# Kernel optimization log

Hardware: AMD Instinct MI355X
Metric: run time of the kernel (lower is better)

## Reference

```python
import jax, jax.numpy as jnp
import numpy as np

DIM_IN = 512
HIDDEN = 512
DIM_OUT = 512
BATCH = 256

def _n_tri(d):
    return (d * d + d) // 2

def _quad_expand(x):
    # x: [B, D] -> [B, D + (D^2+D)/2] with upper-triu (incl diag) pairwise products
    d = x.shape[1]
    iu0, iu1 = np.triu_indices(d)  # static indices
    x_sq = x[:, iu0] * x[:, iu1]  # [B, n_tri] -- avoids materializing full outer
    return jnp.concatenate([x, x_sq], axis=-1)

def setup_inputs() -> dict:
    key = jax.random.key(0)
    k = jax.random.split(key, 5)
    f0 = DIM_IN + _n_tri(DIM_IN)
    f1 = HIDDEN + _n_tri(HIDDEN)
    s0 = 1.0 / np.sqrt(f0)
    s1 = 1.0 / np.sqrt(f1)
    return {
        "x": jax.random.normal(k[0], (BATCH, DIM_IN), dtype=jnp.float32),
        "W0": jax.random.uniform(k[1], (HIDDEN, f0), dtype=jnp.float32, minval=-s0, maxval=s0),
        "b0": jax.random.uniform(k[2], (HIDDEN,), dtype=jnp.float32, minval=-s0, maxval=s0),
        "W1": jax.random.uniform(k[3], (DIM_OUT, f1), dtype=jnp.float32, minval=-s1, maxval=s1),
        "b1": jax.random.uniform(k[4], (DIM_OUT,), dtype=jnp.float32, minval=-s1, maxval=s1),
    }

def reference(x, W0, b0, W1, b1):
    h = _quad_expand(x) @ W0.T + b0  # [B, HIDDEN]
    out = _quad_expand(h) @ W1.T + b1  # [B, DIM_OUT]
    return out
```

## Files before the change

kernel.cpp:

```cpp
#include <hip/hip_runtime.h>

typedef short s16x8 __attribute__((ext_vector_type(8)));
typedef float f32x4 __attribute__((ext_vector_type(4)));

#define DIM     512
#define BATCH   256
#define NTRI    131328
#define FDIM    131840
#define KBLOCKS 2060
#define BN      128
#define NTILES  4
#define CCH     64

__device__ __forceinline__ unsigned short f2bf(float f) {
  __bf16 h = (__bf16)f;
  return __builtin_bit_cast(unsigned short, h);
}
__device__ __forceinline__ float bf2f(unsigned short s) {
  union { unsigned u; float f; } v; v.u = (unsigned)s << 16; return v.f;
}
__device__ __forceinline__ unsigned pk2(float a, float b) {
  return (unsigned)f2bf(a) | ((unsigned)f2bf(b) << 16);
}
__device__ __forceinline__ int swz(int m) { return (m ^ (m >> 2)) & 7; }

__global__ void setup(unsigned* __restrict__ table, const float* __restrict__ x,
                      unsigned short* __restrict__ Xt) {
  int bid = blockIdx.x;
  if (bid < 512) {
    int i = bid;
    int base = i * DIM - (i * (i - 1)) / 2;
    int len = DIM - i;
    for (int t = threadIdx.x; t < len; t += blockDim.x)
      table[base + t] = ((unsigned)i << 16) | (unsigned)(i + t);
  } else {
    int t = (bid - 512) * blockDim.x + threadIdx.x;
    int r = t & (BATCH - 1);
    int c = t >> 8;
    Xt[c * BATCH + r] = f2bf(x[r * DIM + c]);
  }
}

__global__ __launch_bounds__(512)
void featgen(const unsigned* __restrict__ table,
             const unsigned short* __restrict__ Xt,
             uint4* __restrict__ Feat)
{
  const int kb = blockIdx.x;
  const int tid = threadIdx.x;
  const int s8 = tid >> 6;
  const int lane = tid & 63;
  const int f0 = kb * 64 + s8 * 8;
  uint4* out = Feat + ((size_t)kb * 8 + s8) * 256;

  if (f0 < DIM) {
    #pragma unroll
    for (int mb = 0; mb < 4; ++mb) {
      int m = mb * 64 + lane;
      unsigned short v[8];
      #pragma unroll
      for (int e = 0; e < 8; ++e) v[e] = Xt[(f0 + e) * BATCH + m];
      uint4 pk;
      pk.x = (unsigned)v[0] | ((unsigned)v[1] << 16);
      pk.y = (unsigned)v[2] | ((unsigned)v[3] << 16);
      pk.z = (unsigned)v[4] | ((unsigned)v[5] << 16);
      pk.w = (unsigned)v[6] | ((unsigned)v[7] << 16);
      out[m] = pk;
    }
  } else {
    int p0 = f0 - DIM;
    unsigned t0 = table[p0], t7 = table[p0 + 7];
    if ((t0 >> 16) == (t7 >> 16)) {
      int i = (int)(t0 >> 16), j0 = (int)(t0 & 0xffffu);
      #pragma unroll
      for (int mb = 0; mb < 4; ++mb) {
        int m = mb * 64 + lane;
        float xi = bf2f(Xt[i * BATCH + m]);
        float pr[8];
        #pragma unroll
        for (int e = 0; e < 8; ++e) pr[e] = xi * bf2f(Xt[(j0 + e) * BATCH + m]);
        out[m] = make_uint4(pk2(pr[0], pr[1]), pk2(pr[2], pr[3]),
                            pk2(pr[4], pr[5]), pk2(pr[6], pr[7]));
      }
    } else {
      unsigned tt[8];
      #pragma unroll
      for (int e = 0; e < 8; ++e) tt[e] = table[p0 + e];
      #pragma unroll
      for (int mb = 0; mb < 4; ++mb) {
        int m = mb * 64 + lane;
        float pr[8];
        #pragma unroll
        for (int e = 0; e < 8; ++e)
          pr[e] = bf2f(Xt[(tt[e] >> 16) * BATCH + m]) * bf2f(Xt[(tt[e] & 0xffffu) * BATCH + m]);
        out[m] = make_uint4(pk2(pr[0], pr[1]), pk2(pr[2], pr[3]),
                            pk2(pr[4], pr[5]), pk2(pr[6], pr[7]));
      }
    }
  }
}

__global__ __launch_bounds__(512, 2)
void qgemm(const uint4* __restrict__ Feat,
           const float* __restrict__ W,
           unsigned short* __restrict__ partial,
           int C)
{
  __shared__ unsigned short Ws[2][BN * 64];
  const int chunk = blockIdx.x % C;
  const int ntile = blockIdx.x / C;
  const int kb0 = (KBLOCKS * chunk) / C;
  const int kb1 = (KBLOCKS * (chunk + 1)) / C;
  const int n0 = ntile * BN;
  const int tid = threadIdx.x;
  const int lane = tid & 63;
  const int wave = tid >> 6;
  const int wm = wave & 3;
  const int wn = wave >> 2;
  const int lm = lane & 15;
  const int lk = lane >> 4;

  const int wr0 = tid >> 4;
  const int wc16 = tid & 15;

  f32x4 acc[4][4] = {};
  f32x4 wregC[4], wregN[4], wT[4];
  uint4 afrC[4][2], afrN[4][2];

  const float* wp0 = W + (size_t)(n0 + wr0) * FDIM + wc16 * 4;
  const size_t wrow32 = (size_t)32 * FDIM;
  const int abase = lk * 256 + wm * 64 + lm;

  auto loadA = [&](uint4 (*a)[2], int kb) {
    #pragma unroll
    for (int mf = 0; mf < 4; ++mf)
      #pragma unroll
      for (int ks = 0; ks < 2; ++ks)
        a[mf][ks] = Feat[(size_t)kb * 2048 + ks * 1024 + mf * 16 + abase];
  };
  auto loadWr = [&](f32x4* w, int kb) {
    #pragma unroll
    for (int it = 0; it < 4; ++it)
      w[it] = *(const f32x4*)(wp0 + it * wrow32 + (size_t)kb * 64);
  };
  auto storeWs = [&](int buf, const f32x4* w) {
    #pragma unroll
    for (int it = 0; it < 4; ++it) {
      int r = wr0 + it * 32;
      int slot = (wc16 >> 1) ^ swz(r);
      *(uint2*)((char*)&Ws[buf][0] + r * 128 + slot * 16 + (wc16 & 1) * 8) =
          make_uint2(pk2(w[it][0], w[it][1]), pk2(w[it][2], w[it][3]));
    }
  };
  auto compute = [&](int buf, uint4 (*a)[2]) {
    #pragma unroll
    for (int ks = 0; ks < 2; ++ks) {
      s16x8 bfr[4];
      #pragma unroll
      for (int nf = 0; nf < 4; ++nf) {
        int n = wn * 64 + nf * 16 + lm;
        int slot = (ks * 4 + lk) ^ swz(n);
        bfr[nf] = *(const s16x8*)((const char*)&Ws[buf][0] + n * 128 + slot * 16);
      }
      __builtin_amdgcn_s_setprio(1);
      #pragma unroll
      for (int mf = 0; mf < 4; ++mf)
        #pragma unroll
        for (int nf = 0; nf < 4; ++nf)
          acc[mf][nf] = __builtin_amdgcn_mfma_f32_16x16x32_bf16(
              __builtin_bit_cast(s16x8, a[mf][ks]), bfr[nf], acc[mf][nf], 0, 0, 0);
      __builtin_amdgcn_s_setprio(0);
    }
  };

  loadA(afrC, kb0);
  loadWr(wT, kb0);
  loadWr(wregC, min(kb0 + 1, KBLOCKS - 1));
  storeWs(kb0 & 1, wT);
  asm volatile("s_waitcnt lgkmcnt(0)" ::: "memory");
  __builtin_amdgcn_s_barrier();

  for (int kb = kb0; kb < kb1 - 1; ++kb) {
    const int buf = kb & 1;
    loadA(afrN, kb + 1);
    loadWr(wregN, min(kb + 2, KBLOCKS - 1));
    storeWs(buf ^ 1, wregC);
    compute(buf, afrC);
    asm volatile("s_waitcnt lgkmcnt(0)" ::: "memory");
    __builtin_amdgcn_s_barrier();
    #pragma unroll
    for (int mf = 0; mf < 4; ++mf) {
      afrC[mf][0] = afrN[mf][0]; afrC[mf][1] = afrN[mf][1];
    }
    #pragma unroll
    for (int it = 0; it < 4; ++it) wregC[it] = wregN[it];
  }

  compute((kb1 - 1) & 1, afrC);

  unsigned short* pout = partial + (size_t)chunk * (BATCH * DIM);
  #pragma unroll
  for (int mf = 0; mf < 4; ++mf) {
    #pragma unroll
    for (int nf = 0; nf < 4; ++nf) {
      int mrow = wm * 64 + mf * 16 + lk * 4;
      int ncol = n0 + wn * 64 + nf * 16 + lm;
      #pragma unroll
      for (int r = 0; r < 4; ++r)
        pout[(size_t)(mrow + r) * DIM + ncol] = f2bf(acc[mf][nf][r]);
    }
  }
}

__global__ void reduce_h(const unsigned short* __restrict__ partial, const float* __restrict__ bias,
                         unsigned short* __restrict__ Ht, int C) {
  int u = blockIdx.x * blockDim.x + threadIdx.x;
  int t8 = u * 8;
  int b = t8 >> 9;
  int o0 = t8 & (DIM - 1);
  float s[8];
  #pragma unroll
  for (int e = 0; e < 8; ++e) s[e] = bias[o0 + e];
  for (int c = 0; c < C; ++c) {
    uint4 v = *(const uint4*)(partial + (size_t)c * (BATCH * DIM) + t8);
    unsigned w[4] = {v.x, v.y, v.z, v.w};
    #pragma unroll
    for (int p = 0; p < 4; ++p) {
      s[2*p]   += bf2f((unsigned short)(w[p] & 0xffffu));
      s[2*p+1] += bf2f((unsigned short)(w[p] >> 16));
    }
  }
  #pragma unroll
  for (int e = 0; e < 8; ++e)
    Ht[(o0 + e) * BATCH + b] = f2bf(s[e]);
}

__global__ void reduce_out(const unsigned short* __restrict__ partial, const float* __restrict__ bias,
                           float* __restrict__ out, int C) {
  int u = blockIdx.x * blockDim.x + threadIdx.x;
  int t8 = u * 8;
  int o0 = t8 & (DIM - 1);
  float s[8];
  #pragma unroll
  for (int e = 0; e < 8; ++e) s[e] = bias[o0 + e];
  for (int c = 0; c < C; ++c) {
    uint4 v = *(const uint4*)(partial + (size_t)c * (BATCH * DIM) + t8);
    unsigned w[4] = {v.x, v.y, v.z, v.w};
    #pragma unroll
    for (int p = 0; p < 4; ++p) {
      s[2*p]   += bf2f((unsigned short)(w[p] & 0xffffu));
      s[2*p+1] += bf2f((unsigned short)(w[p] >> 16));
    }
  }
  f32x4 lo = {s[0], s[1], s[2], s[3]};
  f32x4 hi = {s[4], s[5], s[6], s[7]};
  *(f32x4*)(out + t8) = lo;
  *(f32x4*)(out + t8 + 4) = hi;
}

extern "C" void kernel_launch(void* const* d_in, const int* in_sizes, int n_in,
                              void* d_out, int out_size, void* d_ws, size_t ws_size,
                              hipStream_t stream) {
  const float* x  = (const float*)d_in[0];
  const float* W0 = (const float*)d_in[1];
  const float* b0 = (const float*)d_in[2];
  const float* W1 = (const float*)d_in[3];
  const float* b1 = (const float*)d_in[4];
  float* out = (float*)d_out;

  char* ws = (char*)d_ws;
  unsigned* table    = (unsigned*)ws;
  unsigned short* Xt = (unsigned short*)(ws + 525312);
  unsigned short* Ht = (unsigned short*)(ws + 787456);
  uint4* Feat        = (uint4*)(ws + 1049600);
  size_t feat_end    = 1049600 + (size_t)KBLOCKS * 32768;
  unsigned short* partial = (unsigned short*)(ws + feat_end);

  size_t avail = (ws_size > feat_end) ? (ws_size - feat_end) : 0;
  int C = (int)(avail / ((size_t)BATCH * DIM * sizeof(unsigned short)));
  if (C > CCH) C = CCH;
  if (C < 1)  C = 1;

  setup<<<dim3(1024), dim3(256), 0, stream>>>(table, x, Xt);

  featgen<<<dim3(KBLOCKS), dim3(512), 0, stream>>>(table, Xt, Feat);
  qgemm<<<dim3(NTILES * C), dim3(512), 0, stream>>>(Feat, W0, partial, C);
  reduce_h<<<dim3(64), dim3(256), 0, stream>>>(partial, b0, Ht, C);

  featgen<<<dim3(KBLOCKS), dim3(512), 0, stream>>>(table, Ht, Feat);
  qgemm<<<dim3(NTILES * C), dim3(512), 0, stream>>>(Feat, W1, partial, C);
  reduce_out<<<dim3(64), dim3(256), 0, stream>>>(partial, b1, out, C);
}
```

Measured before the change: 245.2 us.

## Fuse quadratic feature generation into GEMM with LDS-staged A tiles

Removes the separate featgen pass that wrote the expanded bf16 feature matrix (about 67MB) to global memory. The GEMM now computes the pairwise products on the fly from the transposed input and stages them into shared memory. Blocks grow to 1024 threads with 256-column N tiles and up to 128 K-chunks, so each A tile is generated once per two N tiles instead of being read four times. The cost is more ALU and gather work inside the GEMM loop, more LDS use and lower occupancy.

```diff
diff --git a/kernel.cpp b/kernel.cpp
--- a/kernel.cpp
+++ b/kernel.cpp
@@ -8,9 +8,9 @@
 #define NTRI    131328
 #define FDIM    131840
 #define KBLOCKS 2060
-#define BN      128
-#define NTILES  4
-#define CCH     64
+#define BNW     256
+#define NTILES  2
+#define CCH     128
 
 __device__ __forceinline__ unsigned short f2bf(float f) {
   __bf16 h = (__bf16)f;
@@ -23,6 +23,7 @@
   return (unsigned)f2bf(a) | ((unsigned)f2bf(b) << 16);
 }
 __device__ __forceinline__ int swz(int m) { return (m ^ (m >> 2)) & 7; }
+#define SB() __builtin_amdgcn_sched_barrier(0)
 
 __global__ void setup(unsigned* __restrict__ table, const float* __restrict__ x,
                       unsigned short* __restrict__ Xt) {
@@ -41,77 +42,20 @@
   }
 }
 
-__global__ __launch_bounds__(512)
-void featgen(const unsigned* __restrict__ table,
-             const unsigned short* __restrict__ Xt,
-             uint4* __restrict__ Feat)
-{
-  const int kb = blockIdx.x;
-  const int tid = threadIdx.x;
-  const int s8 = tid >> 6;
-  const int lane = tid & 63;
-  const int f0 = kb * 64 + s8 * 8;
-  uint4* out = Feat + ((size_t)kb * 8 + s8) * 256;
-
-  if (f0 < DIM) {
-    #pragma unroll
-    for (int mb = 0; mb < 4; ++mb) {
-      int m = mb * 64 + lane;
-      unsigned short v[8];
-      #pragma unroll
-      for (int e = 0; e < 8; ++e) v[e] = Xt[(f0 + e) * BATCH + m];
-      uint4 pk;
-      pk.x = (unsigned)v[0] | ((unsigned)v[1] << 16);
-      pk.y = (unsigned)v[2] | ((unsigned)v[3] << 16);
-      pk.z = (unsigned)v[4] | ((unsigned)v[5] << 16);
-      pk.w = (unsigned)v[6] | ((unsigned)v[7] << 16);
-      out[m] = pk;
-    }
-  } else {
-    int p0 = f0 - DIM;
-    unsigned t0 = table[p0], t7 = table[p0 + 7];
-    if ((t0 >> 16) == (t7 >> 16)) {
-      int i = (int)(t0 >> 16), j0 = (int)(t0 & 0xffffu);
-      #pragma unroll
-      for (int mb = 0; mb < 4; ++mb) {
-        int m = mb * 64 + lane;
-        float xi = bf2f(Xt[i * BATCH + m]);
-        float pr[8];
-        #pragma unroll
-        for (int e = 0; e < 8; ++e) pr[e] = xi * bf2f(Xt[(j0 + e) * BATCH + m]);
-        out[m] = make_uint4(pk2(pr[0], pr[1]), pk2(pr[2], pr[3]),
-                            pk2(pr[4], pr[5]), pk2(pr[6], pr[7]));
-      }
-    } else {
-      unsigned tt[8];
-      #pragma unroll
-      for (int e = 0; e < 8; ++e) tt[e] = table[p0 + e];
-      #pragma unroll
-      for (int mb = 0; mb < 4; ++mb) {
-        int m = mb * 64 + lane;
-        float pr[8];
-        #pragma unroll
-        for (int e = 0; e < 8; ++e)
-          pr[e] = bf2f(Xt[(tt[e] >> 16) * BATCH + m]) * bf2f(Xt[(tt[e] & 0xffffu) * BATCH + m]);
-        out[m] = make_uint4(pk2(pr[0], pr[1]), pk2(pr[2], pr[3]),
-                            pk2(pr[4], pr[5]), pk2(pr[6], pr[7]));
-      }
-    }
-  }
-}
-
-__global__ __launch_bounds__(512, 2)
-void qgemm(const uint4* __restrict__ Feat,
+__global__ __launch_bounds__(1024)
+void qgemm(const unsigned* __restrict__ table,
+           const unsigned short* __restrict__ Xt,
            const float* __restrict__ W,
            unsigned short* __restrict__ partial,
            int C)
 {
-  __shared__ unsigned short Ws[2][BN * 64];
+  __shared__ char As[2][8 * 4128];
+  __shared__ unsigned short Ws[2][BNW * 64];
   const int chunk = blockIdx.x % C;
   const int ntile = blockIdx.x / C;
   const int kb0 = (KBLOCKS * chunk) / C;
   const int kb1 = (KBLOCKS * (chunk + 1)) / C;
-  const int n0 = ntile * BN;
+  const int n0 = ntile * BNW;
   const int tid = threadIdx.x;
   const int lane = tid & 63;
   const int wave = tid >> 6;
@@ -122,81 +66,110 @@
 
   const int wr0 = tid >> 4;
   const int wc16 = tid & 15;
+  const int m = tid & 255;
+  const int gb = tid >> 8;
 
   f32x4 acc[4][4] = {};
-  f32x4 wregC[4], wregN[4], wT[4];
-  uint4 afrC[4][2], afrN[4][2];
+  f32x4 wrN[4];
 
   const float* wp0 = W + (size_t)(n0 + wr0) * FDIM + wc16 * 4;
-  const size_t wrow32 = (size_t)32 * FDIM;
-  const int abase = lk * 256 + wm * 64 + lm;
-
-  auto loadA = [&](uint4 (*a)[2], int kb) {
-    #pragma unroll
-    for (int mf = 0; mf < 4; ++mf)
-      #pragma unroll
-      for (int ks = 0; ks < 2; ++ks)
-        a[mf][ks] = Feat[(size_t)kb * 2048 + ks * 1024 + mf * 16 + abase];
+  const size_t wrow64 = (size_t)64 * FDIM;
+
+  auto fgen = [&](int kb, int g) -> uint4 {
+    int f0 = kb * 64 + g * 8;
+    if (f0 < DIM) {
+      unsigned short v[8];
+      #pragma unroll
+      for (int e = 0; e < 8; ++e) v[e] = Xt[(f0 + e) * BATCH + m];
+      return make_uint4((unsigned)v[0] | ((unsigned)v[1] << 16),
+                        (unsigned)v[2] | ((unsigned)v[3] << 16),
+                        (unsigned)v[4] | ((unsigned)v[5] << 16),
+                        (unsigned)v[6] | ((unsigned)v[7] << 16));
+    }
+    int p0 = f0 - DIM;
+    unsigned t0 = table[p0], t7 = table[p0 + 7];
+    float pr[8];
+    if ((t0 >> 16) == (t7 >> 16)) {
+      float xi = bf2f(Xt[(t0 >> 16) * BATCH + m]);
+      int j0 = (int)(t0 & 0xffffu);
+      #pragma unroll
+      for (int e = 0; e < 8; ++e) pr[e] = xi * bf2f(Xt[(j0 + e) * BATCH + m]);
+    } else {
+      #pragma unroll
+      for (int e = 0; e < 8; ++e) {
+        unsigned ij = table[p0 + e];
+        pr[e] = bf2f(Xt[(ij >> 16) * BATCH + m]) * bf2f(Xt[(ij & 0xffffu) * BATCH + m]);
+      }
+    }
+    return make_uint4(pk2(pr[0], pr[1]), pk2(pr[2], pr[3]),
+                      pk2(pr[4], pr[5]), pk2(pr[6], pr[7]));
+  };
+  auto stageA = [&](int kb, int buf) {
+    #pragma unroll
+    for (int p = 0; p < 2; ++p) {
+      int g = gb + 4 * p;
+      uint4 v = fgen(kb, g);
+      *(uint4*)(&As[buf][g * 4128 + m * 16]) = v;
+    }
   };
   auto loadWr = [&](f32x4* w, int kb) {
     #pragma unroll
     for (int it = 0; it < 4; ++it)
-      w[it] = *(const f32x4*)(wp0 + it * wrow32 + (size_t)kb * 64);
+      w[it] = *(const f32x4*)(wp0 + it * wrow64 + (size_t)kb * 64);
   };
   auto storeWs = [&](int buf, const f32x4* w) {
     #pragma unroll
     for (int it = 0; it < 4; ++it) {
-      int r = wr0 + it * 32;
+      int r = wr0 + it * 64;
       int slot = (wc16 >> 1) ^ swz(r);
       *(uint2*)((char*)&Ws[buf][0] + r * 128 + slot * 16 + (wc16 & 1) * 8) =
           make_uint2(pk2(w[it][0], w[it][1]), pk2(w[it][2], w[it][3]));
     }
   };
-  auto compute = [&](int buf, uint4 (*a)[2]) {
+  auto compute = [&](int buf) {
     #pragma unroll
     for (int ks = 0; ks < 2; ++ks) {
-      s16x8 bfr[4];
+      s16x8 bfr[4], afr[4];
       #pragma unroll
       for (int nf = 0; nf < 4; ++nf) {
         int n = wn * 64 + nf * 16 + lm;
         int slot = (ks * 4 + lk) ^ swz(n);
         bfr[nf] = *(const s16x8*)((const char*)&Ws[buf][0] + n * 128 + slot * 16);
       }
+      #pragma unroll
+      for (int mf = 0; mf < 4; ++mf)
+        afr[mf] = *(const s16x8*)(&As[buf][(ks * 4 + lk) * 4128 + (wm * 64 + mf * 16 + lm) * 16]);
       __builtin_amdgcn_s_setprio(1);
       #pragma unroll
       for (int mf = 0; mf < 4; ++mf)
         #pragma unroll
         for (int nf = 0; nf < 4; ++nf)
-          acc[mf][nf] = __builtin_amdgcn_mfma_f32_16x16x32_bf16(
-              __builtin_bit_cast(s16x8, a[mf][ks]), bfr[nf], acc[mf][nf], 0, 0, 0);
+          acc[mf][nf] = __builtin_amdgcn_mfma_f32_16x16x32_bf16(afr[mf], bfr[nf], acc[mf][nf], 0, 0, 0);
       __builtin_amdgcn_s_setprio(0);
     }
   };
 
-  loadA(afrC, kb0);
-  loadWr(wT, kb0);
-  loadWr(wregC, min(kb0 + 1, KBLOCKS - 1));
-  storeWs(kb0 & 1, wT);
-  asm volatile("s_waitcnt lgkmcnt(0)" ::: "memory");
-  __builtin_amdgcn_s_barrier();
+  {
+    f32x4 wT[4];
+    loadWr(wT, kb0);
+    stageA(kb0, 0);
+    storeWs(0, wT);
+    loadWr(wrN, min(kb0 + 1, KBLOCKS - 1));
+    asm volatile("s_waitcnt lgkmcnt(0)" ::: "memory"); SB();
+    __builtin_amdgcn_s_barrier();
+  }
 
   for (int kb = kb0; kb < kb1 - 1; ++kb) {
-    const int buf = kb & 1;
-    loadA(afrN, kb + 1);
-    loadWr(wregN, min(kb + 2, KBLOCKS - 1));
-    storeWs(buf ^ 1, wregC);
-    compute(buf, afrC);
-    asm volatile("s_waitcnt lgkmcnt(0)" ::: "memory");
+    const int buf = (kb - kb0) & 1;
+    stageA(kb + 1, buf ^ 1);
+    storeWs(buf ^ 1, wrN);
+    loadWr(wrN, min(kb + 2, KBLOCKS - 1));
+    compute(buf);
+    asm volatile("s_waitcnt lgkmcnt(0)" ::: "memory"); SB();
     __builtin_amdgcn_s_barrier();
-    #pragma unroll
-    for (int mf = 0; mf < 4; ++mf) {
-      afrC[mf][0] = afrN[mf][0]; afrC[mf][1] = afrN[mf][1];
-    }
-    #pragma unroll
-    for (int it = 0; it < 4; ++it) wregC[it] = wregN[it];
-  }
-
-  compute((kb1 - 1) & 1, afrC);
+  }
+
+  compute((kb1 - 1 - kb0) & 1);
 
   unsigned short* pout = partial + (size_t)chunk * (BATCH * DIM);
   #pragma unroll
@@ -272,22 +245,18 @@
   unsigned* table    = (unsigned*)ws;
   unsigned short* Xt = (unsigned short*)(ws + 525312);
   unsigned short* Ht = (unsigned short*)(ws + 787456);
-  uint4* Feat        = (uint4*)(ws + 1049600);
-  size_t feat_end    = 1049600 + (size_t)KBLOCKS * 32768;
-  unsigned short* partial = (unsigned short*)(ws + feat_end);
-
-  size_t avail = (ws_size > feat_end) ? (ws_size - feat_end) : 0;
+  unsigned short* partial = (unsigned short*)(ws + 1049600);
+
+  size_t avail = (ws_size > 1049600) ? (ws_size - 1049600) : 0;
   int C = (int)(avail / ((size_t)BATCH * DIM * sizeof(unsigned short)));
   if (C > CCH) C = CCH;
   if (C < 1)  C = 1;
 
   setup<<<dim3(1024), dim3(256), 0, stream>>>(table, x, Xt);
 
-  featgen<<<dim3(KBLOCKS), dim3(512), 0, stream>>>(table, Xt, Feat);
-  qgemm<<<dim3(NTILES * C), dim3(512), 0, stream>>>(Feat, W0, partial, C);
+  qgemm<<<dim3(NTILES * C), dim3(1024), 0, stream>>>(table, Xt, W0, partial, C);
   reduce_h<<<dim3(64), dim3(256), 0, stream>>>(partial, b0, Ht, C);
 
-  featgen<<<dim3(KBLOCKS), dim3(512), 0, stream>>>(table, Ht, Feat);
-  qgemm<<<dim3(NTILES * C), dim3(512), 0, stream>>>(Feat, W1, partial, C);
+  qgemm<<<dim3(NTILES * C), dim3(1024), 0, stream>>>(table, Ht, W1, partial, C);
   reduce_out<<<dim3(64), dim3(256), 0, stream>>>(partial, b1, out, C);
 }
```

After: 395.6 us. 61.3% more time.
